# Performance work log

Hardware: AMD Instinct MI355X
Metric: run time of the kernel (lower is better)

The kernel has to match this reference:

```python
import jax, jax.numpy as jnp
import numpy as np

M = 64; N_SC = 32; SPS = 8; LENCP = 16; NUMOFDM = 256 // N_SC
BETA = 0.5; SPAN = 16; LENRRC = SPAN * SPS + 1  # 129
FC = 25e6; FS = 10e6 * SPS
CLIP = 1.2; SNR = 10.0; THRES = 8.0
LEN_T = NUMOFDM * (M + LENCP)              # 640
NUMSAMPLES = LEN_T * SPS + LENRRC * 2      # 5378
L1 = LEN_T * SPS + LENRRC - 1              # 5248 (post pulse-shaping length)


def make_rrc():
    # standard root-raised-cosine, unit energy
    t = np.arange(-SPAN * SPS // 2, SPAN * SPS // 2 + 1) / SPS
    h = np.zeros_like(t)
    eps = 1e-9
    t0 = np.abs(t) < eps
    ts = np.abs(np.abs(t) - 1.0 / (4 * BETA)) < eps
    reg = ~(t0 | ts)
    tr = t[reg]
    h[reg] = (np.sin(np.pi * tr * (1 - BETA)) + 4 * BETA * tr * np.cos(np.pi * tr * (1 + BETA))) / (
        np.pi * tr * (1 - (4 * BETA * tr) ** 2))
    h[t0] = 1 + BETA * (4 / np.pi - 1)
    h[ts] = (BETA / np.sqrt(2)) * ((1 + 2 / np.pi) * np.sin(np.pi / (4 * BETA)) +
                                   (1 - 2 / np.pi) * np.cos(np.pi / (4 * BETA)))
    h = h / np.sqrt(np.sum(h ** 2))
    return h.astype(np.float32)


def _conv_full(u, k):
    # torch F.conv1d(x, k.flip(), padding=K-1) == full convolution with k
    K = k.shape[0]
    return jax.lax.conv_general_dilated(
        u[:, None, :], k[::-1][None, None, :], (1,), [(K - 1, K - 1)],
        dimension_numbers=('NCH', 'OIH', 'NCH'))[:, 0, :]


def _pulse_filter(c, rrc):
    return _conv_full(c.real, rrc) + 1j * _conv_full(c.imag, rrc)


def _power_norm(z):
    m = jnp.mean(z, axis=1, keepdims=True)
    s = jnp.std(z, axis=1, ddof=1, keepdims=True)  # torch.std is unbiased
    return (z - m) / (s + 1e-8)


def _forward(x, W_enc, b_enc, W_dec, b_dec, rrc, awgn, startloc):
    B = x.shape[0]
    # --- encoder (linear proxy for ResNetTx) -> 512 reals ---
    z = x.reshape(B, -1) @ W_enc + b_enc
    z = _power_norm(z)
    c = z.reshape(B, 256, 2)
    c = (c[..., 0] + 1j * c[..., 1]).reshape(B, NUMOFDM, N_SC)  # complex64
    # --- DFT precoding ---
    c = jnp.fft.fftshift(jnp.fft.fft(c, axis=-1, norm='ortho'), axes=-1)
    # --- subcarrier mapping (contiguous block, mapping==1) ---
    loc = jnp.arange(startloc, startloc + N_SC)
    data_f = jnp.zeros((B, NUMOFDM, M), jnp.complex64).at[:, :, loc].set(c)
    data_t = jnp.fft.ifft(data_f, axis=-1, norm='ortho')
    data_t = jnp.concatenate([data_t[:, :, -LENCP:], data_t], axis=-1)  # CP
    data_t = data_t.reshape(B, LEN_T)
    # --- zero-stuffed upsampling + RRC pulse shaping ---
    over = jnp.zeros((B, LEN_T * SPS), jnp.complex64).at[:, ::SPS].set(data_t)
    xc = _pulse_filter(over, rrc)  # (B, L1)
    # --- carrier mixing ---
    n = jnp.arange(NUMSAMPLES, dtype=jnp.float32)
    cos_c = jnp.sqrt(2.0) * jnp.cos(2 * jnp.pi * FC * n / FS)
    sin_c = jnp.sqrt(2.0) * jnp.sin(2 * jnp.pi * FC * n / FS)
    data_x = xc.real * cos_c[:L1] - xc.imag * sin_c[:L1]
    # --- clipping ---
    thr = CLIP * jnp.sqrt(jnp.mean(jnp.square(data_x), axis=1, keepdims=True))
    over_amp = jax.nn.relu(jnp.abs(data_x) - thr)
    data_x = (1.0 - over_amp / (jnp.abs(data_x) + 1e-8)) * data_x
    # --- PAPR ---
    tstart = (LENRRC + 1) // 2
    p = jnp.square(data_x[:, tstart:tstart + LEN_T * SPS])
    PAPRdB = 10.0 * jnp.log10(jnp.max(p, axis=1) / jnp.mean(p, axis=1))
    PAPRloss = jnp.mean(jax.nn.relu(PAPRdB - THRES))
    # --- AWGN channel (no fading) ---
    data_r = data_x + awgn
    # --- downconversion + matched filter ---
    rc = data_r * cos_c[:L1] - 1j * (data_r * sin_c[:L1])
    filt = _pulse_filter(rc, rrc)  # (B, L1 + LENRRC - 1) = (B, 5376)
    y = filt[:, LENRRC - 1:filt.shape[1] - LENRRC:SPS]  # (B, LEN_T)
    y = y.reshape(B, NUMOFDM, M + LENCP)[:, :, LENCP:]
    y = jnp.fft.fft(y, axis=-1, norm='ortho')[:, :, loc]
    y = jnp.fft.ifft(jnp.fft.fftshift(y, axes=-1), axis=-1, norm='ortho')
    y = y.reshape(B, NUMOFDM * N_SC)
    y = jnp.stack([y.real, y.imag], axis=-1).reshape(B, 8, 8, 8)
    # --- decoder (linear proxy for ResNetRx) ---
    out = (y.reshape(B, 512) @ W_dec + b_dec).reshape(B, 3, 32, 32)
    return out, PAPRdB, PAPRloss


def setup_inputs() -> dict:
    key = jax.random.key(0)
    ks = jax.random.split(key, 4)
    B = 1024
    x = jax.random.normal(ks[0], (B, 3, 32, 32), jnp.float32)
    W_enc = jax.random.normal(ks[1], (3072, 512), jnp.float32) * 0.02
    b_enc = jnp.zeros((512,), jnp.float32)
    W_dec = jax.random.normal(ks[2], (512, 3072), jnp.float32) * 0.05
    b_dec = jnp.zeros((3072,), jnp.float32)
    rrc = jnp.asarray(make_rrc())
    noise_std = 10.0 ** (-SNR / 20.0)
    awgn = jax.random.normal(ks[3], (B, L1), jnp.float32) * noise_std
    return {"x": x, "W_enc": W_enc, "b_enc": b_enc, "W_dec": W_dec,
            "b_dec": b_dec, "rrc": rrc, "awgn": awgn, "startloc": 7}


def reference(x, W_enc, b_enc, W_dec, b_dec, rrc, awgn, startloc):
    return _forward(x, W_enc, b_enc, W_dec, b_dec, rrc, awgn, startloc)
```

## Files before the change

kernel.cpp:

```cpp
#include <hip/hip_runtime.h>
#include <hip/hip_bf16.h>
#include <math.h>

#define L1_     5248
#define LENRRC_ 129
#define TSTART_ 65
#define NWIN_   5120
#define SWZ(m) ((m) + ((m) >> 3))

typedef __attribute__((ext_vector_type(8))) short s16x8;
typedef __attribute__((ext_vector_type(4))) float f32x4;

__device__ inline ushort bf16_rne(float x) {
    unsigned xb = __float_as_uint(x);
    return (ushort)((xb + 0x7fffu + ((xb >> 16) & 1u)) >> 16);
}

__device__ inline float wave_sum(float v) {
    #pragma unroll
    for (int m = 32; m > 0; m >>= 1) v += __shfl_xor(v, m, 64);
    return v;
}
__device__ inline float wave_max(float v) {
    #pragma unroll
    for (int m = 32; m > 0; m >>= 1) v = fmaxf(v, __shfl_xor(v, m, 64));
    return v;
}

__device__ inline void gl_lds16(const void* g, void* l) {
    __builtin_amdgcn_global_load_lds(
        (const __attribute__((address_space(1))) unsigned int*)g,
        (__attribute__((address_space(3))) unsigned int*)l, 16, 0, 0);
}

__global__ __launch_bounds__(256) void pack_k(const float* __restrict__ x,
        const float* __restrict__ W1, const float* __restrict__ W2,
        const float* __restrict__ benc,
        ushort* __restrict__ xb, ushort* __restrict__ w1t, ushort* __restrict__ w2t,
        float* __restrict__ z)
{
    __shared__ ushort tile[64][70];
    const int blk = blockIdx.x, tid = threadIdx.x;
    if (blk < 3072) {
        int i = blk * 256 + tid;
        float4 v = ((const float4*)x)[i];
        ushort4 h;
        h.x = bf16_rne(v.x); h.y = bf16_rne(v.y);
        h.z = bf16_rne(v.z); h.w = bf16_rne(v.w);
        ((ushort4*)xb)[i] = h;
    } else if (blk < 3840) {
        const float* W; ushort* T; int K, N, n0, k0;
        if (blk < 3456) {
            int idx = blk - 3072;
            W = W1; T = w1t; K = 3072; N = 512;
            n0 = (idx & 7) * 64; k0 = (idx >> 3) * 64;
        } else {
            int idx = blk - 3456;
            W = W2; T = w2t; K = 512; N = 3072;
            n0 = (idx % 48) * 64; k0 = (idx / 48) * 64;
        }
        const int cr = tid >> 4, cc = (tid & 15) * 4;
        #pragma unroll
        for (int i = 0; i < 4; ++i) {
            int kk = i * 16 + cr;
            float4 v = *(const float4*)&W[(size_t)(k0 + kk) * N + n0 + cc];
            tile[kk][cc]     = bf16_rne(v.x);
            tile[kk][cc + 1] = bf16_rne(v.y);
            tile[kk][cc + 2] = bf16_rne(v.z);
            tile[kk][cc + 3] = bf16_rne(v.w);
        }
        __syncthreads();
        #pragma unroll
        for (int i = 0; i < 4; ++i) {
            int nn = i * 16 + cr;
            ushort4 h;
            h.x = tile[cc][nn]; h.y = tile[cc + 1][nn];
            h.z = tile[cc + 2][nn]; h.w = tile[cc + 3][nn];
            *(ushort4*)&T[(size_t)(n0 + nn) * K + k0 + cc] = h;
        }
    } else {
        int i = (blk - 3840) * 256 + tid;
        z[i] = benc[i & 511];
    }
}

__global__ __launch_bounds__(256) void gemm1_k(const ushort* __restrict__ Ab,
        const ushort* __restrict__ Bb, float* __restrict__ C, int M, int N, int K,
        int partial)
{
    __shared__ __attribute__((aligned(16))) ushort Asl[64 * 64];
    __shared__ __attribute__((aligned(16))) ushort Bsl[128 * 64];
    const int tid = threadIdx.x;
    const int lane = tid & 63, wave = tid >> 6;
    const int wm = (wave >> 1) * 32, wn = (wave & 1) * 64;
    const int m0 = blockIdx.y * 64, n0 = blockIdx.x * 128;
    const int kch = K / 8, kbeg = blockIdx.z * kch, kend = kbeg + kch;
    const int fm = lane & 15, q = lane >> 4;
    f32x4 acc[2][4] = {};

    int arow[2], akb[2], brow[4], bkb[4];
    #pragma unroll
    for (int j = 0; j < 2; ++j) {
        int c = ((wave * 2 + j) << 6) + lane;
        arow[j] = c >> 3; akb[j] = (c & 7) ^ (arow[j] & 7);
    }
    #pragma unroll
    for (int j = 0; j < 4; ++j) {
        int c = ((wave * 4 + j) << 6) + lane;
        brow[j] = c >> 3; bkb[j] = (c & 7) ^ (brow[j] & 7);
    }

    for (int kt = kbeg; kt < kend; kt += 64) {
        #pragma unroll
        for (int j = 0; j < 2; ++j)
            gl_lds16(&Ab[(size_t)(m0 + arow[j]) * K + kt + akb[j] * 8],
                     &Asl[(wave * 2 + j) << 9]);
        #pragma unroll
        for (int j = 0; j < 4; ++j)
            gl_lds16(&Bb[(size_t)(n0 + brow[j]) * K + kt + bkb[j] * 8],
                     &Bsl[(wave * 4 + j) << 9]);
        __syncthreads();
        #pragma unroll
        for (int ks = 0; ks < 2; ++ks) {
            s16x8 a[2], b[4];
            #pragma unroll
            for (int mf = 0; mf < 2; ++mf) {
                int r = wm + mf * 16 + fm;
                a[mf] = *(const s16x8*)&Asl[(r << 6) + ((((ks << 2) + q) ^ (r & 7)) << 3)];
            }
            #pragma unroll
            for (int nf = 0; nf < 4; ++nf) {
                int r = wn + nf * 16 + fm;
                b[nf] = *(const s16x8*)&Bsl[(r << 6) + ((((ks << 2) + q) ^ (r & 7)) << 3)];
            }
            #pragma unroll
            for (int mf = 0; mf < 2; ++mf)
                #pragma unroll
                for (int nf = 0; nf < 4; ++nf)
                    acc[mf][nf] = __builtin_amdgcn_mfma_f32_16x16x32_bf16(a[mf], b[nf], acc[mf][nf], 0, 0, 0);
        }
        __syncthreads();
    }

    if (partial) {
        float* Cs = C + (size_t)blockIdx.z * ((size_t)M * N);
        #pragma unroll
        for (int mf = 0; mf < 2; ++mf)
            #pragma unroll
            for (int nf = 0; nf < 4; ++nf)
                #pragma unroll
                for (int r = 0; r < 4; ++r) {
                    int m = m0 + wm + mf * 16 + q * 4 + r;
                    int n = n0 + wn + nf * 16 + fm;
                    Cs[(size_t)m * N + n] = acc[mf][nf][r];
                }
    } else {
        #pragma unroll
        for (int mf = 0; mf < 2; ++mf)
            #pragma unroll
            for (int nf = 0; nf < 4; ++nf)
                #pragma unroll
                for (int r = 0; r < 4; ++r) {
                    int m = m0 + wm + mf * 16 + q * 4 + r;
                    int n = n0 + wn + nf * 16 + fm;
                    atomicAdd(&C[(size_t)m * N + n], acc[mf][nf][r]);
                }
    }
}

__global__ __launch_bounds__(256) void gemm2_k(const ushort* __restrict__ Ab,
        const ushort* __restrict__ Bb, const float* __restrict__ bias,
        const float* __restrict__ papr, float* __restrict__ C,
        float* __restrict__ out_loss, int M, int N, int K)
{
    __shared__ __attribute__((aligned(16))) ushort Asl[64 * 64];
    __shared__ __attribute__((aligned(16))) ushort Bsl[64 * 64];
    __shared__ float red[4];
    const int tid = threadIdx.x;
    const int lane = tid & 63, wave = tid >> 6;
    const int wm = (wave >> 1) * 32, wn = (wave & 1) * 32;
    const int m0 = blockIdx.y * 64, n0 = blockIdx.x * 64;
    const int fm = lane & 15, q = lane >> 4;
    f32x4 acc[2][2] = {};

    int srow[2], skb[2];
    #pragma unroll
    for (int j = 0; j < 2; ++j) {
        int c = ((wave * 2 + j) << 6) + lane;
        srow[j] = c >> 3; skb[j] = (c & 7) ^ (srow[j] & 7);
    }

    for (int kt = 0; kt < K; kt += 64) {
        #pragma unroll
        for (int j = 0; j < 2; ++j) {
            gl_lds16(&Ab[(size_t)(m0 + srow[j]) * K + kt + skb[j] * 8],
                     &Asl[(wave * 2 + j) << 9]);
            gl_lds16(&Bb[(size_t)(n0 + srow[j]) * K + kt + skb[j] * 8],
                     &Bsl[(wave * 2 + j) << 9]);
        }
        __syncthreads();
        #pragma unroll
        for (int ks = 0; ks < 2; ++ks) {
            s16x8 a[2], b[2];
            #pragma unroll
            for (int mf = 0; mf < 2; ++mf) {
                int r = wm + mf * 16 + fm;
                a[mf] = *(const s16x8*)&Asl[(r << 6) + ((((ks << 2) + q) ^ (r & 7)) << 3)];
            }
            #pragma unroll
            for (int nf = 0; nf < 2; ++nf) {
                int r = wn + nf * 16 + fm;
                b[nf] = *(const s16x8*)&Bsl[(r << 6) + ((((ks << 2) + q) ^ (r & 7)) << 3)];
            }
            #pragma unroll
            for (int mf = 0; mf < 2; ++mf)
                #pragma unroll
                for (int nf = 0; nf < 2; ++nf)
                    acc[mf][nf] = __builtin_amdgcn_mfma_f32_16x16x32_bf16(a[mf], b[nf], acc[mf][nf], 0, 0, 0);
        }
        __syncthreads();
    }

    #pragma unroll
    for (int mf = 0; mf < 2; ++mf)
        #pragma unroll
        for (int nf = 0; nf < 2; ++nf)
            #pragma unroll
            for (int r = 0; r < 4; ++r) {
                int m = m0 + wm + mf * 16 + q * 4 + r;
                int n = n0 + wn + nf * 16 + fm;
                C[(size_t)m * N + n] = acc[mf][nf][r] + bias[n];
            }

    if (blockIdx.x == 0 && blockIdx.y == 0) {
        float s = 0.f;
        for (int i = tid; i < 1024; i += 256) { float v = papr[i] - 8.f; s += v > 0.f ? v : 0.f; }
        s = wave_sum(s);
        if (lane == 0) red[wave] = s;
        __syncthreads();
        if (tid == 0) *out_loss = (red[0] + red[1] + red[2] + red[3]) * (1.f / 1024.f);
    }
}

__global__ __launch_bounds__(256, 4) void mega_k(const float* __restrict__ z,
        const float* __restrict__ benc,
        const float* __restrict__ rrc, const float* __restrict__ awgn,
        const int* __restrict__ slocp, ushort* __restrict__ y5b,
        float* __restrict__ papr, float* __restrict__ out_papr, int nsp)
{
    __shared__ float  zl[512];
    __shared__ float2 frfi[8][32];
    __shared__ float2 trti[672];
    __shared__ float  hl[132];
    __shared__ float  csl[16], ssl[16];
    __shared__ float2 cs64[64];
    __shared__ float2 gcs[130];
    __shared__ float  dxr[SWZ(L1_ - 1) + 1];
    __shared__ float2 wrli[512];
    __shared__ float  red[4], red2[4];

    const int b = blockIdx.x, tid = threadIdx.x;
    const int lane = tid & 63, wv = tid >> 6;
    const int sloc = *slocp;

    if (tid < 64) {
        float ang = 0.09817477042468103f * (float)tid;
        float s, c; sincosf(ang, &s, &c);
        cs64[tid] = make_float2(c, s);
    }
    if (tid >= 64 && tid < 80) {
        int t = tid - 64;
        float ang = 1.9634954084936207f * (float)t;
        float s, c; sincosf(ang, &s, &c);
        csl[t] = 1.4142135623730951f * c; ssl[t] = 1.4142135623730951f * s;
    }
    if (tid >= 96 && tid < 128) {
        int t = tid - 96;
        int idx = (t < 16) ? t : (640 + t);
        trti[idx] = make_float2(0.f, 0.f);
    }
    for (int e = tid; e < LENRRC_; e += 256) hl[e] = rrc[e];

    float v0, v1;
    if (nsp) {
        v0 = benc[tid]; v1 = benc[tid + 256];
        const float* zp = z + (size_t)b * 512;
        #pragma unroll
        for (int s = 0; s < 8; ++s) {
            v0 += zp[(size_t)s * 524288 + tid];
            v1 += zp[(size_t)s * 524288 + tid + 256];
        }
    } else {
        v0 = z[(size_t)b * 512 + tid];
        v1 = z[(size_t)b * 512 + tid + 256];
    }
    __syncthreads();

    if (tid < LENRRC_) {
        int neg = (16 - (tid & 15)) & 15;
        gcs[tid] = make_float2(hl[tid] * csl[neg], hl[tid] * ssl[neg]);
    }

    {
        float S = wave_sum(v0 + v1);
        float Q = wave_sum(v0 * v0 + v1 * v1);
        if (lane == 0) { red[wv] = S; red2[wv] = Q; }
    }
    __syncthreads();
    {
        float S = red[0] + red[1] + red[2] + red[3];
        float Q = red2[0] + red2[1] + red2[2] + red2[3];
        float mean = S * (1.f / 512.f);
        float var = (Q - S * mean) * (1.f / 511.f);
        float inv = 1.f / (sqrtf(var) + 1e-8f);
        zl[tid] = (v0 - mean) * inv; zl[tid + 256] = (v1 - mean) * inv;
    }
    __syncthreads();

    {
        int s = tid >> 5, kk = tid & 31;
        int kk2 = (kk + 16) & 31;
        float sr = 0.f, si = 0.f;
        int t2 = 0;
        #pragma unroll 4
        for (int q = 0; q < 32; ++q) {
            float2 w = cs64[2 * t2];
            float2 c = *(const float2*)&zl[(s * 32 + q) * 2];
            sr += c.x * w.x + c.y * w.y;
            si += c.y * w.x - c.x * w.y;
            t2 = (t2 + kk2) & 31;
        }
        frfi[s][kk] = make_float2(sr * 0.1767766952966369f, si * 0.1767766952966369f);
    }
    __syncthreads();

    {
        int s = tid >> 5, n = tid & 31;
        float er = 0.f, ei = 0.f, or_ = 0.f, oi = 0.f;
        int t = (sloc * n) & 63;
        #pragma unroll 2
        for (int k = 0; k < 32; k += 2) {
            float2 w = cs64[t];
            float2 f = frfi[s][k];
            er += f.x * w.x - f.y * w.y;
            ei += f.y * w.x + f.x * w.y;
            t = (t + n) & 63;
            w = cs64[t];
            f = frfi[s][k + 1];
            or_ += f.x * w.x - f.y * w.y;
            oi  += f.y * w.x + f.x * w.y;
            t = (t + n) & 63;
        }
        float sgn = (sloc & 1) ? -1.f : 1.f;
        float dr0 = (er + or_) * 0.125f, di0 = (ei + oi) * 0.125f;
        float dr1 = sgn * (er - or_) * 0.125f, di1 = sgn * (ei - oi) * 0.125f;
        int base = s * 80;
        trti[base + 32 + n] = make_float2(dr0, di0);
        trti[base + 64 + n] = make_float2(dr1, di1);
        if (n >= 16) trti[base + n] = make_float2(dr1, di1);
    }
    __syncthreads();

    float ss = 0.f;
    for (int a = tid; a < 656; a += 256) {
        float accr[8] = {}, acci[8] = {};
        #pragma unroll 4
        for (int d = 0; d < 16; ++d) {
            float2 tv = trti[16 + a - d];
            #pragma unroll
            for (int r = 0; r < 8; ++r) {
                float h = hl[r + 8 * d];
                accr[r] += tv.x * h; acci[r] += tv.y * h;
            }
        }
        {
            float2 tv = trti[a];
            float h = hl[128];
            accr[0] += tv.x * h; acci[0] += tv.y * h;
        }
        int cb = (a & 1) * 8;
        #pragma unroll
        for (int r = 0; r < 8; ++r) {
            float v = accr[r] * csl[cb + r] - acci[r] * ssl[cb + r];
            dxr[SWZ(a * 8 + r)] = v;
            ss += v * v;
        }
    }
    ss = wave_sum(ss);
    if (lane == 0) red[wv] = ss;
    __syncthreads();
    float thr = 1.2f * sqrtf((red[0] + red[1] + red[2] + red[3]) / (float)L1_);
    __syncthreads();

    float pmax = 0.f, psum = 0.f;
    {
        const float4* ag = (const float4*)&awgn[(size_t)b * L1_];
        for (int ii = tid; ii < 1312; ii += 256) {
            float4 aw = ag[ii];
            int i = ii * 4;
            #pragma unroll
            for (int e = 0; e < 4; ++e) {
                int idx = i + e;
                float x = dxr[SWZ(idx)];
                float ax = fabsf(x);
                float over = fmaxf(ax - thr, 0.f);
                float y = (1.f - over / (ax + 1e-8f)) * x;
                if (idx >= TSTART_ && idx < TSTART_ + NWIN_) {
                    float p = y * y; psum += p; pmax = fmaxf(pmax, p);
                }
                float awv = (e == 0) ? aw.x : (e == 1) ? aw.y : (e == 2) ? aw.z : aw.w;
                dxr[SWZ(idx)] = y + awv;
            }
        }
    }
    psum = wave_sum(psum); pmax = wave_max(pmax);
    if (lane == 0) { red[wv] = psum; red2[wv] = pmax; }
    __syncthreads();
    if (tid == 0) {
        float sum = red[0] + red[1] + red[2] + red[3];
        float mx = fmaxf(fmaxf(red2[0], red2[1]), fmaxf(red2[2], red2[3]));
        float pdb = 10.f * log10f(mx / (sum / (float)NWIN_));
        papr[b] = pdb;
        out_papr[b] = pdb;
    }
    __syncthreads();

    {
        int s = tid >> 6, n = tid & 63;
        int T0 = s * 80 + n + 32;
        int base0 = 9 * T0;
        int base1 = 9 * (T0 + 320);
        float ar0 = 0.f, ai0 = 0.f, ar1 = 0.f, ai1 = 0.f;
        int db = 0;
        #pragma unroll 2
        for (int e = 0; e < 16; ++e) {
            #pragma unroll
            for (int u = 0; u < 8; ++u) {
                int off = (u == 0) ? 0 : (u + 1);
                float2 g = gcs[db + u];
                float va = dxr[base0 - off];
                float vb = dxr[base1 - off];
                ar0 += va * g.x; ai0 += va * g.y;
                ar1 += vb * g.x; ai1 += vb * g.y;
            }
            base0 -= 9; base1 -= 9; db += 8;
        }
        {
            float2 g = gcs[128];
            float va = dxr[base0], vb = dxr[base1];
            ar0 += va * g.x; ai0 += va * g.y;
            ar1 += vb * g.x; ai1 += vb * g.y;
        }
        bool odd = (n & 1);
        wrli[tid]       = make_float2(odd ? -ar0 : ar0, odd ? ai0 : -ai0);
        wrli[tid + 256] = make_float2(odd ? -ar1 : ar1, odd ? ai1 : -ai1);
    }
    __syncthreads();

    {
        int s = tid >> 5, n = tid & 31;
        float2 d0 = wrli[s * 64 + n];
        float2 d1 = wrli[s * 64 + n + 32];
        trti[s * 32 + n]       = make_float2(d0.x + d1.x, d0.y + d1.y);
        trti[256 + s * 32 + n] = make_float2(d0.x - d1.x, d0.y - d1.y);
    }
    __syncthreads();

    {
        int s = tid >> 5, kk = tid & 31;
        int f = sloc + kk;
        const float2* dsel = &trti[((f & 1) ? 256 : 0) + s * 32];
        float vr = 0.f, vi = 0.f;
        int t = 0;
        #pragma unroll 4
        for (int n = 0; n < 32; ++n) {
            float2 w = cs64[t];
            float2 d = dsel[n];
            vr += d.x * w.x + d.y * w.y;
            vi += d.y * w.x - d.x * w.y;
            t = (t + f) & 63;
        }
        int ksh = (kk + 16) & 31;
        frfi[s][ksh] = make_float2(vr * 0.125f, vi * 0.125f);
    }
    __syncthreads();

    {
        int s = tid >> 5, q2 = tid & 31;
        float ur = 0.f, ui = 0.f;
        int t2 = 0;
        #pragma unroll 4
        for (int k = 0; k < 32; ++k) {
            float2 w = cs64[2 * t2];
            float2 f = frfi[s][k];
            ur += f.x * w.x - f.y * w.y;
            ui += f.y * w.x + f.x * w.y;
            t2 = (t2 + q2) & 31;
        }
        ur *= 0.1767766952966369f; ui *= 0.1767766952966369f;
        ushort2 hv; hv.x = bf16_rne(ur); hv.y = bf16_rne(ui);
        *(ushort2*)&y5b[(size_t)b * 512 + (s * 32 + q2) * 2] = hv;
    }
}

extern "C" void kernel_launch(void* const* d_in, const int* in_sizes, int n_in,
                              void* d_out, int out_size, void* d_ws, size_t ws_size,
                              hipStream_t stream) {
    const float* x    = (const float*)d_in[0];
    const float* Wenc = (const float*)d_in[1];
    const float* benc = (const float*)d_in[2];
    const float* Wdec = (const float*)d_in[3];
    const float* bdec = (const float*)d_in[4];
    const float* rrc  = (const float*)d_in[5];
    const float* awgn = (const float*)d_in[6];
    const int* sloc   = (const int*)d_in[7];
    float* out = (float*)d_out;

    char* wsb = (char*)d_ws;
    ushort* xb   = (ushort*)wsb;                     wsb += (size_t)1024 * 3072 * 2;
    ushort* w1t  = (ushort*)wsb;                     wsb += (size_t)512 * 3072 * 2;
    ushort* w2t  = (ushort*)wsb;                     wsb += (size_t)3072 * 512 * 2;
    ushort* y5b  = (ushort*)wsb;                     wsb += (size_t)1024 * 512 * 2;
    float*  papr = (float*)wsb;                      wsb += 1024 * 4;
    float*  zbuf = (float*)wsb;
    size_t head = (size_t)((char*)zbuf - (char*)d_ws);
    int partial = (ws_size >= head + (size_t)8 * 1024 * 512 * 4) ? 1 : 0;

    float* out_papr = out + (size_t)1024 * 3072;
    float* out_loss = out_papr + 1024;

    pack_k<<<partial ? 3840 : 5888, 256, 0, stream>>>(x, Wenc, Wdec, benc, xb, w1t, w2t, zbuf);
    gemm1_k<<<dim3(4, 16, 8), 256, 0, stream>>>(xb, w1t, zbuf, 1024, 512, 3072, partial);
    mega_k<<<1024, 256, 0, stream>>>(zbuf, benc, rrc, awgn, sloc, y5b, papr, out_papr,
                                     partial ? 8 : 0);
    gemm2_k<<<dim3(48, 16, 1), 256, 0, stream>>>(y5b, w2t, bdec, papr, out, out_loss, 1024, 3072, 512);
}
```

Before: 147.2 us.

## Double mega_k block size to 512 threads and split per-thread work

The per-sample mega kernel now launches 512 threads instead of 256. Each thread handles one z element, one matched-filter output, and half the pulse-shaping work, so per-thread register pressure drops and each block exposes more parallelism. Several stages (the DFTs) still use only 256 threads and leave half the block idle, and the reductions now span 8 waves. The launch bound of 512 threads with 8 blocks per CU may force a tight register cap, and shared memory per block limits residency in any case.

```diff
diff --git a/kernel.cpp b/kernel.cpp
--- a/kernel.cpp
+++ b/kernel.cpp
@@ -242,7 +242,7 @@
     }
 }
 
-__global__ __launch_bounds__(256, 4) void mega_k(const float* __restrict__ z,
+__global__ __launch_bounds__(512, 8) void mega_k(const float* __restrict__ z,
         const float* __restrict__ benc,
         const float* __restrict__ rrc, const float* __restrict__ awgn,
         const int* __restrict__ slocp, ushort* __restrict__ y5b,
@@ -257,7 +257,7 @@
     __shared__ float2 gcs[130];
     __shared__ float  dxr[SWZ(L1_ - 1) + 1];
     __shared__ float2 wrli[512];
-    __shared__ float  red[4], red2[4];
+    __shared__ float  red[8], red2[8];
 
     const int b = blockIdx.x, tid = threadIdx.x;
     const int lane = tid & 63, wv = tid >> 6;
@@ -279,20 +279,18 @@
         int idx = (t < 16) ? t : (640 + t);
         trti[idx] = make_float2(0.f, 0.f);
     }
-    for (int e = tid; e < LENRRC_; e += 256) hl[e] = rrc[e];
-
-    float v0, v1;
+    if (tid < LENRRC_ + 256 && tid >= 256) hl[tid - 256] = rrc[tid - 256];
+    if (tid >= 128 && tid < 131) hl[tid] = 0.f;
+
+    float v0;
     if (nsp) {
-        v0 = benc[tid]; v1 = benc[tid + 256];
+        v0 = benc[tid];
         const float* zp = z + (size_t)b * 512;
         #pragma unroll
-        for (int s = 0; s < 8; ++s) {
+        for (int s = 0; s < 8; ++s)
             v0 += zp[(size_t)s * 524288 + tid];
-            v1 += zp[(size_t)s * 524288 + tid + 256];
-        }
     } else {
         v0 = z[(size_t)b * 512 + tid];
-        v1 = z[(size_t)b * 512 + tid + 256];
     }
     __syncthreads();
 
@@ -302,22 +300,23 @@
     }
 
     {
-        float S = wave_sum(v0 + v1);
-        float Q = wave_sum(v0 * v0 + v1 * v1);
+        float S = wave_sum(v0);
+        float Q = wave_sum(v0 * v0);
         if (lane == 0) { red[wv] = S; red2[wv] = Q; }
     }
     __syncthreads();
     {
-        float S = red[0] + red[1] + red[2] + red[3];
-        float Q = red2[0] + red2[1] + red2[2] + red2[3];
+        float S = 0.f, Q = 0.f;
+        #pragma unroll
+        for (int w = 0; w < 8; ++w) { S += red[w]; Q += red2[w]; }
         float mean = S * (1.f / 512.f);
         float var = (Q - S * mean) * (1.f / 511.f);
         float inv = 1.f / (sqrtf(var) + 1e-8f);
-        zl[tid] = (v0 - mean) * inv; zl[tid + 256] = (v1 - mean) * inv;
-    }
-    __syncthreads();
-
-    {
+        zl[tid] = (v0 - mean) * inv;
+    }
+    __syncthreads();
+
+    if (tid < 256) {
         int s = tid >> 5, kk = tid & 31;
         int kk2 = (kk + 16) & 31;
         float sr = 0.f, si = 0.f;
@@ -334,7 +333,7 @@
     }
     __syncthreads();
 
-    {
+    if (tid < 256) {
         int s = tid >> 5, n = tid & 31;
         float er = 0.f, ei = 0.f, or_ = 0.f, oi = 0.f;
         int t = (sloc * n) & 63;
@@ -362,40 +361,50 @@
     __syncthreads();
 
     float ss = 0.f;
-    for (int a = tid; a < 656; a += 256) {
-        float accr[8] = {}, acci[8] = {};
-        #pragma unroll 4
-        for (int d = 0; d < 16; ++d) {
-            float2 tv = trti[16 + a - d];
-            #pragma unroll
-            for (int r = 0; r < 8; ++r) {
-                float h = hl[r + 8 * d];
-                accr[r] += tv.x * h; acci[r] += tv.y * h;
-            }
-        }
-        {
-            float2 tv = trti[a];
-            float h = hl[128];
-            accr[0] += tv.x * h; acci[0] += tv.y * h;
-        }
+    for (int a = tid; a < 656; a += 512) {
         int cb = (a & 1) * 8;
         #pragma unroll
-        for (int r = 0; r < 8; ++r) {
-            float v = accr[r] * csl[cb + r] - acci[r] * ssl[cb + r];
-            dxr[SWZ(a * 8 + r)] = v;
-            ss += v * v;
+        for (int g = 0; g < 2; ++g) {
+            float accr[4] = {}, acci[4] = {};
+            #pragma unroll 4
+            for (int d = 0; d < 16; ++d) {
+                float2 tv = trti[16 + a - d];
+                #pragma unroll
+                for (int r = 0; r < 4; ++r) {
+                    float h = hl[g * 4 + r + 8 * d];
+                    accr[r] += tv.x * h; acci[r] += tv.y * h;
+                }
+            }
+            if (g == 0) {
+                float2 tv = trti[a];
+                float h = hl[128];
+                accr[0] += tv.x * h; acci[0] += tv.y * h;
+            }
+            #pragma unroll
+            for (int r = 0; r < 4; ++r) {
+                int rr = g * 4 + r;
+                float v = accr[r] * csl[cb + rr] - acci[r] * ssl[cb + rr];
+                dxr[SWZ(a * 8 + rr)] = v;
+                ss += v * v;
+            }
         }
     }
     ss = wave_sum(ss);
     if (lane == 0) red[wv] = ss;
     __syncthreads();
-    float thr = 1.2f * sqrtf((red[0] + red[1] + red[2] + red[3]) / (float)L1_);
+    float thr;
+    {
+        float S = 0.f;
+        #pragma unroll
+        for (int w = 0; w < 8; ++w) S += red[w];
+        thr = 1.2f * sqrtf(S / (float)L1_);
+    }
     __syncthreads();
 
     float pmax = 0.f, psum = 0.f;
     {
         const float4* ag = (const float4*)&awgn[(size_t)b * L1_];
-        for (int ii = tid; ii < 1312; ii += 256) {
+        for (int ii = tid; ii < 1312; ii += 512) {
             float4 aw = ag[ii];
             int i = ii * 4;
             #pragma unroll
@@ -417,8 +426,9 @@
     if (lane == 0) { red[wv] = psum; red2[wv] = pmax; }
     __syncthreads();
     if (tid == 0) {
-        float sum = red[0] + red[1] + red[2] + red[3];
-        float mx = fmaxf(fmaxf(red2[0], red2[1]), fmaxf(red2[2], red2[3]));
+        float sum = 0.f, mx = 0.f;
+        #pragma unroll
+        for (int w = 0; w < 8; ++w) { sum += red[w]; mx = fmaxf(mx, red2[w]); }
         float pdb = 10.f * log10f(mx / (sum / (float)NWIN_));
         papr[b] = pdb;
         out_papr[b] = pdb;
@@ -428,45 +438,42 @@
     {
         int s = tid >> 6, n = tid & 63;
         int T0 = s * 80 + n + 32;
-        int base0 = 9 * T0;
-        int base1 = 9 * (T0 + 320);
-        float ar0 = 0.f, ai0 = 0.f, ar1 = 0.f, ai1 = 0.f;
+        int base = 9 * T0;
+        float ar = 0.f, ai = 0.f;
         int db = 0;
-        #pragma unroll 2
+        #pragma unroll 4
         for (int e = 0; e < 16; ++e) {
             #pragma unroll
             for (int u = 0; u < 8; ++u) {
                 int off = (u == 0) ? 0 : (u + 1);
                 float2 g = gcs[db + u];
-                float va = dxr[base0 - off];
-                float vb = dxr[base1 - off];
-                ar0 += va * g.x; ai0 += va * g.y;
-                ar1 += vb * g.x; ai1 += vb * g.y;
-            }
-            base0 -= 9; base1 -= 9; db += 8;
+                float va = dxr[base - off];
+                ar += va * g.x; ai += va * g.y;
+            }
+            base -= 9; db += 8;
         }
         {
             float2 g = gcs[128];
-            float va = dxr[base0], vb = dxr[base1];
-            ar0 += va * g.x; ai0 += va * g.y;
-            ar1 += vb * g.x; ai1 += vb * g.y;
+            float va = dxr[base];
+            ar += va * g.x; ai += va * g.y;
         }
         bool odd = (n & 1);
-        wrli[tid]       = make_float2(odd ? -ar0 : ar0, odd ? ai0 : -ai0);
-        wrli[tid + 256] = make_float2(odd ? -ar1 : ar1, odd ? ai1 : -ai1);
+        wrli[tid] = make_float2(odd ? -ar : ar, odd ? ai : -ai);
     }
     __syncthreads();
 
     {
-        int s = tid >> 5, n = tid & 31;
+        int h = tid >> 8, r = tid & 255;
+        int s = r >> 5, n = r & 31;
         float2 d0 = wrli[s * 64 + n];
         float2 d1 = wrli[s * 64 + n + 32];
-        trti[s * 32 + n]       = make_float2(d0.x + d1.x, d0.y + d1.y);
-        trti[256 + s * 32 + n] = make_float2(d0.x - d1.x, d0.y - d1.y);
-    }
-    __syncthreads();
-
-    {
+        float2 v = h ? make_float2(d0.x - d1.x, d0.y - d1.y)
+                     : make_float2(d0.x + d1.x, d0.y + d1.y);
+        trti[h * 256 + s * 32 + n] = v;
+    }
+    __syncthreads();
+
+    if (tid < 256) {
         int s = tid >> 5, kk = tid & 31;
         int f = sloc + kk;
         const float2* dsel = &trti[((f & 1) ? 256 : 0) + s * 32];
@@ -485,7 +492,7 @@
     }
     __syncthreads();
 
-    {
+    if (tid < 256) {
         int s = tid >> 5, q2 = tid & 31;
         float ur = 0.f, ui = 0.f;
         int t2 = 0;
@@ -531,7 +538,7 @@
 
     pack_k<<<partial ? 3840 : 5888, 256, 0, stream>>>(x, Wenc, Wdec, benc, xb, w1t, w2t, zbuf);
     gemm1_k<<<dim3(4, 16, 8), 256, 0, stream>>>(xb, w1t, zbuf, 1024, 512, 3072, partial);
-    mega_k<<<1024, 256, 0, stream>>>(zbuf, benc, rrc, awgn, sloc, y5b, papr, out_papr,
+    mega_k<<<1024, 512, 0, stream>>>(zbuf, benc, rrc, awgn, sloc, y5b, papr, out_papr,
                                      partial ? 8 : 0);
     gemm2_k<<<dim3(48, 16, 1), 256, 0, stream>>>(y5b, w2t, bdec, papr, out, out_loss, 1024, 3072, 512);
 }
```

Result: no change. 148.9 us (+1.2%).
